# Kernel tuning notes

Hardware: AMD Instinct MI355X
Metric: run time of the kernel (lower is better)

The kernel has to match this reference:

```python
import jax, jax.numpy as jnp
import numpy as np

N_GENE = 100000
N_DIS = 20000
H = 128
E = 500000


def setup_inputs() -> dict:
    key = jax.random.key(0)
    ks = jax.random.split(key, 12)
    s1 = 1.0 / np.sqrt(2 * H)  # fan-in init scale, Linear(2H, H)
    s2 = 1.0 / np.sqrt(H)      # fan-in init scale, Linear(H, 1)
    z_gene = jax.random.normal(ks[0], (N_GENE, H), jnp.float32)
    z_disease = jax.random.normal(ks[1], (N_DIS, H), jnp.float32)
    # gene->disease edges: row indexes genes, col indexes diseases
    edges_gd = jnp.stack([
        jax.random.randint(ks[2], (E,), 0, N_GENE),
        jax.random.randint(ks[3], (E,), 0, N_DIS),
    ])
    # gene->gene edges
    edges_gg = jnp.stack([
        jax.random.randint(ks[4], (E,), 0, N_GENE),
        jax.random.randint(ks[5], (E,), 0, N_GENE),
    ])
    return {
        "z_gene": z_gene,
        "z_disease": z_disease,
        "edges_gd": edges_gd,
        "edges_gg": edges_gg,
        "w1_gd": jax.random.normal(ks[6], (2 * H, H), jnp.float32) * s1,
        "b1_gd": jnp.zeros((H,), jnp.float32),
        "w2_gd": jax.random.normal(ks[7], (H, 1), jnp.float32) * s2,
        "b2_gd": jnp.zeros((1,), jnp.float32),
        "w1_gg": jax.random.normal(ks[8], (2 * H, H), jnp.float32) * s1,
        "b1_gg": jnp.zeros((H,), jnp.float32),
        "w2_gg": jax.random.normal(ks[9], (H, 1), jnp.float32) * s2,
        "b2_gg": jnp.zeros((1,), jnp.float32),
    }


def _decode(z_src, z_dst, edges, w1, b1, w2, b2):
    # gather src/dst node embeddings by edge index, concat -> [E, 2H]
    z = jnp.concatenate([z_src[edges[0]], z_dst[edges[1]]], axis=1)
    h = jnp.maximum(z @ w1 + b1, 0.0)  # Linear + ReLU
    return h @ w2 + b2                  # Linear -> [E, 1]


def reference(z_gene, z_disease, edges_gd, edges_gg,
              w1_gd, b1_gd, w2_gd, b2_gd,
              w1_gg, b1_gg, w2_gg, b2_gg):
    out_gd = _decode(z_gene, z_disease, edges_gd, w1_gd, b1_gd, w2_gd, b2_gd)
    out_gg = _decode(z_gene, z_gene, edges_gg, w1_gg, b1_gg, w2_gg, b2_gg)
    # dict of per-relation outputs in the original; stack since E matches
    return jnp.stack([out_gd, out_gg])  # [2, E, 1]
```

## Files before the change

kernel.cpp:

```cpp
#include <hip/hip_runtime.h>
#include <hip/hip_bf16.h>

#define HDIM 128

typedef __attribute__((ext_vector_type(8))) short short8;
typedef __attribute__((ext_vector_type(4))) float floatx4;

__device__ __forceinline__ float bf2f(unsigned short u) {
    return __uint_as_float(((unsigned)u) << 16);
}
__device__ __forceinline__ unsigned short f2b(float f) {
    __hip_bfloat16 h = __float2bfloat16(f);
    return __builtin_bit_cast(unsigned short, h);
}
__device__ __forceinline__ float ldv(const void* p, size_t i, int flag) {
    return flag ? bf2f(((const unsigned short*)p)[i]) : ((const float*)p)[i];
}
__device__ __forceinline__ short8 pack8(float4 a, float4 b) {
    short8 r;
    r[0] = (short)f2b(a.x); r[1] = (short)f2b(a.y);
    r[2] = (short)f2b(a.z); r[3] = (short)f2b(a.w);
    r[4] = (short)f2b(b.x); r[5] = (short)f2b(b.y);
    r[6] = (short)f2b(b.z); r[7] = (short)f2b(b.w);
    return r;
}

__device__ __forceinline__ int local_detect(const unsigned short* zbits) {
    __shared__ int red[256];
    int tid = threadIdx.x;
    int cnt = 0;
    for (int i = tid; i < 4096; i += 256) {
        int ex = (zbits[i] >> 7) & 0xFF;
        if (ex >= 100 && ex <= 140) cnt++;
    }
    red[tid] = cnt;
    __syncthreads();
    for (int s = 128; s > 0; s >>= 1) {
        if (tid < s) red[tid] += red[tid + s];
        __syncthreads();
    }
    return (red[0] >= 3686) ? 1 : 0;
}

__global__ __launch_bounds__(256) void prep_kernel(
    const unsigned short* __restrict__ zbits,
    const void* __restrict__ w1_gd, const void* __restrict__ w1_gg,
    const void* __restrict__ b1_gd, const void* __restrict__ w2_gd,
    const void* __restrict__ b2_gd, const void* __restrict__ b1_gg,
    const void* __restrict__ w2_gg, const void* __restrict__ b2_gg,
    unsigned short* __restrict__ img, float* __restrict__ params,
    int* __restrict__ flagout)
{
    int flag = local_detect(zbits);
    int b = blockIdx.x;
    int tid = threadIdx.x;
    if (b < 32) {
        int im   = b >> 3;
        int sub  = b & 7;
        const void* w1 = (im < 2) ? w1_gd : w1_gg;
        int part = im & 1;
        unsigned short* out = img + im * 16384;
        int n = tid & 127;
#pragma unroll
        for (int it = 0; it < 8; ++it) {
            int k = sub * 16 + it * 2 + (tid >> 7);
            unsigned short v = flag
                ? ((const unsigned short*)w1)[(size_t)(part * 128 + k) * 128 + n]
                : f2b(((const float*)w1)[(size_t)(part * 128 + k) * 128 + n]);
            out[n * 128 + (((k >> 3) ^ (n & 15)) << 3) + (k & 7)] = v;
        }
    } else {
        if (tid < 128) {
            params[tid]       = ldv(b1_gd, tid, flag);
            params[256 + tid] = ldv(b1_gg, tid, flag);
        } else {
            params[tid]       = ldv(w2_gd, tid - 128, flag);
            params[256 + tid] = ldv(w2_gg, tid - 128, flag);
        }
        if (tid == 0) {
            params[512] = ldv(b2_gd, 0, flag);
            params[513] = ldv(b2_gg, 0, flag);
            *flagout = flag;
        }
    }
}

__global__ __launch_bounds__(256) void proj_all_kernel(
    const void* __restrict__ Zg, const void* __restrict__ Zd,
    const uint4* __restrict__ Wimg, const float* __restrict__ params,
    unsigned short* __restrict__ A_gd, unsigned short* __restrict__ B_gd,
    unsigned short* __restrict__ A_gg, unsigned short* __restrict__ B_gg,
    int NG, int ND, int gblk, const int* __restrict__ flagp)
{
    __shared__ uint4 sW[2048];
    int tid  = threadIdx.x;
    int lane = tid & 63;
    int wave = tid >> 6;
    int nl   = lane & 15;
    int quad = lane >> 4;
    int flag = *flagp;

    bool gene = (int)blockIdx.x < gblk;
    int blk = gene ? blockIdx.x : blockIdx.x - gblk;
    int M = gene ? NG : ND;
    const void* Z = gene ? Zg : Zd;

    int row0 = blk * 128 + wave * 32 + nl;
    int row1 = row0 + 16;
    int r0c = row0 < M ? row0 : (M - 1);
    int r1c = row1 < M ? row1 : (M - 1);

    short8 zf[2][4];
    if (flag) {
        const uint4* z0 = (const uint4*)Z + (size_t)r0c * 16;
        const uint4* z1 = (const uint4*)Z + (size_t)r1c * 16;
#pragma unroll
        for (int kc = 0; kc < 4; ++kc) {
            zf[0][kc] = __builtin_bit_cast(short8, z0[kc * 4 + quad]);
            zf[1][kc] = __builtin_bit_cast(short8, z1[kc * 4 + quad]);
        }
    } else {
        const float4* z0 = (const float4*)Z + (size_t)r0c * 32;
        const float4* z1 = (const float4*)Z + (size_t)r1c * 32;
#pragma unroll
        for (int kc = 0; kc < 4; ++kc) {
            int o = kc * 8 + quad * 2;
            zf[0][kc] = pack8(z0[o], z0[o + 1]);
            zf[1][kc] = pack8(z1[o], z1[o + 1]);
        }
    }

    int nph = gene ? 3 : 1;
    for (int ph = 0; ph < nph; ++ph) {
        const uint4* im;
        unsigned short* Out;
        const float* bias;
        if (gene) {
            im   = Wimg + (ph == 0 ? 0 : ph == 1 ? 2 : 3) * 2048;
            Out  = ph == 0 ? A_gd : ph == 1 ? A_gg : B_gg;
            bias = ph == 0 ? params : ph == 1 ? params + 256 : nullptr;
        } else {
            im = Wimg + 2048; Out = B_gd; bias = nullptr;
        }
        __syncthreads();
#pragma unroll
        for (int i = 0; i < 8; ++i) sW[tid + i * 256] = im[tid + i * 256];
        __syncthreads();

        floatx4 acc[2][8];
#pragma unroll
        for (int rt = 0; rt < 2; ++rt)
#pragma unroll
            for (int nt = 0; nt < 8; ++nt)
                acc[rt][nt] = (floatx4){0.f, 0.f, 0.f, 0.f};

#pragma unroll
        for (int kc = 0; kc < 4; ++kc) {
            int p = (kc * 4 + quad) ^ nl;
#pragma unroll
            for (int nt = 0; nt < 8; ++nt) {
                short8 wf = __builtin_bit_cast(short8, sW[(nt * 16 + nl) * 16 + p]);
                acc[0][nt] = __builtin_amdgcn_mfma_f32_16x16x32_bf16(wf, zf[0][kc], acc[0][nt], 0, 0, 0);
                acc[1][nt] = __builtin_amdgcn_mfma_f32_16x16x32_bf16(wf, zf[1][kc], acc[1][nt], 0, 0, 0);
            }
        }
#pragma unroll
        for (int rt = 0; rt < 2; ++rt) {
            int row = rt ? row1 : row0;
            if (row < M) {
#pragma unroll
                for (int nt = 0; nt < 8; ++nt) {
                    float4 bv = {0.f, 0.f, 0.f, 0.f};
                    if (bias) bv = *(const float4*)(bias + nt * 16 + quad * 4);
                    ushort4 v;
                    v.x = f2b(acc[rt][nt][0] + bv.x);
                    v.y = f2b(acc[rt][nt][1] + bv.y);
                    v.z = f2b(acc[rt][nt][2] + bv.z);
                    v.w = f2b(acc[rt][nt][3] + bv.w);
                    *(ushort4*)(Out + (size_t)row * HDIM + nt * 16 + quad * 4) = v;
                }
            }
        }
    }
}

__global__ __launch_bounds__(256) void edge_kernel(
    const int* __restrict__ edges_gd, const int* __restrict__ edges_gg,
    const unsigned short* __restrict__ A_gd, const unsigned short* __restrict__ B_gd,
    const unsigned short* __restrict__ A_gg, const unsigned short* __restrict__ B_gg,
    const float* __restrict__ params,
    void* __restrict__ out, int E, int nb, const int* __restrict__ flagp)
{
    int rel = ((int)blockIdx.x >= nb) ? 1 : 0;
    int blk = blockIdx.x - rel * nb;
    const int* edges = rel ? edges_gg : edges_gd;
    const unsigned short* A = rel ? A_gg : A_gd;
    const unsigned short* B = rel ? B_gg : B_gd;
    const float* w2 = params + 128 + rel * 256;
    float b2 = params[512 + rel];

    int tid  = threadIdx.x;
    int lane = tid & 63;
    int wave = tid >> 6;
    int nl   = lane & 7;
    int grp  = lane >> 3;

    float w2f[16];
#pragma unroll
    for (int i = 0; i < 4; ++i) {
        float4 t = *(const float4*)(w2 + nl * 16 + i * 4);
        w2f[i * 4 + 0] = t.x; w2f[i * 4 + 1] = t.y;
        w2f[i * 4 + 2] = t.z; w2f[i * 4 + 3] = t.w;
    }

    int e0 = blk * 64 + (wave * 8 + grp) * 2;
    int e1 = e0 + 1;
    int emax = E - 2 > 0 ? E - 2 : 0;
    int ec = e0 < emax ? e0 : emax;
    int sel = e0 - ec;
    int2 sp = *(const int2*)(edges + ec);
    int2 dp = *(const int2*)(edges + E + ec);
    int src0 = sel ? sp.y : sp.x;
    int dst0 = sel ? dp.y : dp.x;
    int src1 = sp.y;
    int dst1 = dp.y;

    const uint4* a0p = (const uint4*)(A + (size_t)src0 * HDIM) + nl * 2;
    const uint4* b0p = (const uint4*)(B + (size_t)dst0 * HDIM) + nl * 2;
    const uint4* a1p = (const uint4*)(A + (size_t)src1 * HDIM) + nl * 2;
    const uint4* b1p = (const uint4*)(B + (size_t)dst1 * HDIM) + nl * 2;
    uint4 a0[2] = {a0p[0], a0p[1]};
    uint4 c0[2] = {b0p[0], b0p[1]};
    uint4 a1[2] = {a1p[0], a1p[1]};
    uint4 c1[2] = {b1p[0], b1p[1]};

    float acc0 = 0.f, acc1 = 0.f;
#pragma unroll
    for (int i = 0; i < 2; ++i) {
        const unsigned* au0 = (const unsigned*)&a0[i];
        const unsigned* cu0 = (const unsigned*)&c0[i];
        const unsigned* au1 = (const unsigned*)&a1[i];
        const unsigned* cu1 = (const unsigned*)&c1[i];
#pragma unroll
        for (int j = 0; j < 4; ++j) {
            int ch = i * 8 + j * 2;
            float x0 = __uint_as_float(au0[j] << 16);
            float x1 = __uint_as_float(au0[j] & 0xffff0000u);
            float y0 = __uint_as_float(cu0[j] << 16);
            float y1 = __uint_as_float(cu0[j] & 0xffff0000u);
            acc0 = fmaf(fmaxf(x0 + y0, 0.f), w2f[ch], acc0);
            acc0 = fmaf(fmaxf(x1 + y1, 0.f), w2f[ch + 1], acc0);
            float u0 = __uint_as_float(au1[j] << 16);
            float u1 = __uint_as_float(au1[j] & 0xffff0000u);
            float v0 = __uint_as_float(cu1[j] << 16);
            float v1 = __uint_as_float(cu1[j] & 0xffff0000u);
            acc1 = fmaf(fmaxf(u0 + v0, 0.f), w2f[ch], acc1);
            acc1 = fmaf(fmaxf(u1 + v1, 0.f), w2f[ch + 1], acc1);
        }
    }
    acc0 += __shfl_xor(acc0, 1); acc1 += __shfl_xor(acc1, 1);
    acc0 += __shfl_xor(acc0, 2); acc1 += __shfl_xor(acc1, 2);
    acc0 += __shfl_xor(acc0, 4); acc1 += __shfl_xor(acc1, 4);

    if (nl == 0) {
        int flag = *flagp;
        size_t base = (size_t)rel * E;
        if (e0 < E) {
            float r = acc0 + b2;
            if (flag) ((unsigned short*)out)[base + e0] = f2b(r);
            else      ((float*)out)[base + e0] = r;
        }
        if (e1 < E) {
            float r = acc1 + b2;
            if (flag) ((unsigned short*)out)[base + e1] = f2b(r);
            else      ((float*)out)[base + e1] = r;
        }
    }
}

__global__ __launch_bounds__(256) void detect_kernel(
    const unsigned short* __restrict__ zbits, int* __restrict__ flag)
{
    int f = local_detect(zbits);
    if (threadIdx.x == 0) *flag = f;
}

__global__ __launch_bounds__(128) void naive_edge_kernel(
    const int* __restrict__ edges,
    const void* __restrict__ zsrc, const void* __restrict__ zdst,
    const void* __restrict__ w1, const void* __restrict__ b1,
    const void* __restrict__ w2, const void* __restrict__ b2,
    void* __restrict__ out, size_t eoff, int E,
    const int* __restrict__ flagp)
{
    int flag = flagp ? *flagp : 0;
    __shared__ float zs[128], zd[128], red[128];
    int e = blockIdx.x;
    int n = threadIdx.x;
    int src = edges[e], dst = edges[E + e];
    zs[n] = ldv(zsrc, (size_t)src * HDIM + n, flag);
    zd[n] = ldv(zdst, (size_t)dst * HDIM + n, flag);
    __syncthreads();
    float acc = ldv(b1, n, flag);
    for (int k = 0; k < 128; ++k) acc = fmaf(zs[k], ldv(w1, (size_t)k * HDIM + n, flag), acc);
    for (int k = 0; k < 128; ++k) acc = fmaf(zd[k], ldv(w1, (size_t)(128 + k) * HDIM + n, flag), acc);
    red[n] = fmaxf(acc, 0.f) * ldv(w2, n, flag);
    __syncthreads();
    for (int s = 64; s > 0; s >>= 1) {
        if (n < s) red[n] += red[n + s];
        __syncthreads();
    }
    if (n == 0) {
        float r = red[0] + ldv(b2, 0, flag);
        if (flag) ((unsigned short*)out)[eoff + e] = f2b(r);
        else      ((float*)out)[eoff + e] = r;
    }
}

extern "C" void kernel_launch(void* const* d_in, const int* in_sizes, int n_in,
                              void* d_out, int out_size, void* d_ws, size_t ws_size,
                              hipStream_t stream)
{
    const void* z_gene = d_in[0];
    const void* z_dis  = d_in[1];
    const int* edges_gd = (const int*)d_in[2];
    const int* edges_gg = (const int*)d_in[3];
    const void* w1_gd = d_in[4];
    const void* b1_gd = d_in[5];
    const void* w2_gd = d_in[6];
    const void* b2_gd = d_in[7];
    const void* w1_gg = d_in[8];
    const void* b1_gg = d_in[9];
    const void* w2_gg = d_in[10];
    const void* b2_gg = d_in[11];

    int NG = in_sizes[0] / HDIM;
    int ND = in_sizes[1] / HDIM;
    int E  = in_sizes[2] / 2;

    size_t off_flag   = 0;
    size_t off_params = 256;
    size_t off_img    = 2560;
    size_t off_Agd    = off_img + 131072;
    size_t off_Bgd    = off_Agd + (size_t)NG * HDIM * 2;
    size_t off_Agg    = off_Bgd + (size_t)ND * HDIM * 2;
    size_t off_Bgg    = off_Agg + (size_t)NG * HDIM * 2;
    size_t need       = off_Bgg + (size_t)NG * HDIM * 2;

    char* ws = (char*)d_ws;

    if (ws_size < need) {
        const int* flagp = nullptr;
        if (ws_size >= 16) {
            detect_kernel<<<1, 256, 0, stream>>>((const unsigned short*)z_gene, (int*)ws);
            flagp = (const int*)ws;
        }
        naive_edge_kernel<<<E, 128, 0, stream>>>(edges_gd, z_gene, z_dis,
                                                 w1_gd, b1_gd, w2_gd, b2_gd,
                                                 d_out, 0, E, flagp);
        naive_edge_kernel<<<E, 128, 0, stream>>>(edges_gg, z_gene, z_gene,
                                                 w1_gg, b1_gg, w2_gg, b2_gg,
                                                 d_out, (size_t)E, E, flagp);
        return;
    }

    int* flag = (int*)(ws + off_flag);
    float* params = (float*)(ws + off_params);
    unsigned short* img = (unsigned short*)(ws + off_img);
    unsigned short* Agd = (unsigned short*)(ws + off_Agd);
    unsigned short* Bgd = (unsigned short*)(ws + off_Bgd);
    unsigned short* Agg = (unsigned short*)(ws + off_Agg);
    unsigned short* Bgg = (unsigned short*)(ws + off_Bgg);

    prep_kernel<<<33, 256, 0, stream>>>((const unsigned short*)z_gene,
                                        w1_gd, w1_gg, b1_gd, w2_gd, b2_gd,
                                        b1_gg, w2_gg, b2_gg, img, params, flag);

    const uint4* img4 = (const uint4*)img;
    int gblk = (NG + 127) / 128;
    int dblk = (ND + 127) / 128;
    proj_all_kernel<<<gblk + dblk, 256, 0, stream>>>(z_gene, z_dis, img4, params,
                                                     Agd, Bgd, Agg, Bgg,
                                                     NG, ND, gblk, flag);

    int nb = (E + 63) / 64;
    edge_kernel<<<2 * nb, 256, 0, stream>>>(edges_gd, edges_gg, Agd, Bgd, Agg, Bgg,
                                            params, d_out, E, nb, flag);
}
```

Baseline: 226.6 us.

## Split projection into per-matrix blocks reading weights directly from global memory

Replaces the fused projection kernel, which reused one loaded z tile across three weight phases via a swizzled LDS image, with one block per (matrix, 64-row tile). Weight fragments are read directly from global/L2 in a plain layout, removing LDS staging and barriers, and a zero bias region replaces the null-bias branch. This raises parallelism and removes synchronisation but re-reads gene embeddings three times and relies on L2 for weight loads.

```diff
diff --git a/kernel.cpp b/kernel.cpp
--- a/kernel.cpp
+++ b/kernel.cpp
@@ -67,12 +67,13 @@
             unsigned short v = flag
                 ? ((const unsigned short*)w1)[(size_t)(part * 128 + k) * 128 + n]
                 : f2b(((const float*)w1)[(size_t)(part * 128 + k) * 128 + n]);
-            out[n * 128 + (((k >> 3) ^ (n & 15)) << 3) + (k & 7)] = v;
+            out[n * 128 + k] = v;
         }
     } else {
         if (tid < 128) {
             params[tid]       = ldv(b1_gd, tid, flag);
             params[256 + tid] = ldv(b1_gg, tid, flag);
+            params[768 + tid] = 0.f;
         } else {
             params[tid]       = ldv(w2_gd, tid - 128, flag);
             params[256 + tid] = ldv(w2_gg, tid - 128, flag);
@@ -85,101 +86,68 @@
     }
 }
 
-__global__ __launch_bounds__(256) void proj_all_kernel(
+__global__ __launch_bounds__(256) void proj_kernel(
     const void* __restrict__ Zg, const void* __restrict__ Zd,
-    const uint4* __restrict__ Wimg, const float* __restrict__ params,
+    const uint4* __restrict__ img, const float* __restrict__ params,
     unsigned short* __restrict__ A_gd, unsigned short* __restrict__ B_gd,
     unsigned short* __restrict__ A_gg, unsigned short* __restrict__ B_gg,
     int NG, int ND, int gblk, const int* __restrict__ flagp)
 {
-    __shared__ uint4 sW[2048];
+    int id = blockIdx.x;
+    const void* Z; int M; const uint4* W; unsigned short* Out; const float* bias;
+    if (id < gblk)            { Z = Zg; M = NG; W = img;            Out = A_gd; bias = params;       }
+    else if (id < 2 * gblk)   { Z = Zg; M = NG; W = img + 2 * 2048; Out = A_gg; bias = params + 256; id -= gblk; }
+    else if (id < 3 * gblk)   { Z = Zg; M = NG; W = img + 3 * 2048; Out = B_gg; bias = params + 768; id -= 2 * gblk; }
+    else                      { Z = Zd; M = ND; W = img + 2048;     Out = B_gd; bias = params + 768; id -= 3 * gblk; }
+
     int tid  = threadIdx.x;
     int lane = tid & 63;
     int wave = tid >> 6;
     int nl   = lane & 15;
     int quad = lane >> 4;
-    int flag = *flagp;
-
-    bool gene = (int)blockIdx.x < gblk;
-    int blk = gene ? blockIdx.x : blockIdx.x - gblk;
-    int M = gene ? NG : ND;
-    const void* Z = gene ? Zg : Zd;
-
-    int row0 = blk * 128 + wave * 32 + nl;
-    int row1 = row0 + 16;
-    int r0c = row0 < M ? row0 : (M - 1);
-    int r1c = row1 < M ? row1 : (M - 1);
-
-    short8 zf[2][4];
-    if (flag) {
-        const uint4* z0 = (const uint4*)Z + (size_t)r0c * 16;
-        const uint4* z1 = (const uint4*)Z + (size_t)r1c * 16;
-#pragma unroll
-        for (int kc = 0; kc < 4; ++kc) {
-            zf[0][kc] = __builtin_bit_cast(short8, z0[kc * 4 + quad]);
-            zf[1][kc] = __builtin_bit_cast(short8, z1[kc * 4 + quad]);
-        }
+
+    int row = id * 64 + wave * 16 + nl;
+    int rc  = row < M ? row : (M - 1);
+
+    short8 zf[4];
+    if (*flagp) {
+        const uint4* z = (const uint4*)Z + (size_t)rc * 16;
+#pragma unroll
+        for (int kc = 0; kc < 4; ++kc)
+            zf[kc] = __builtin_bit_cast(short8, z[kc * 4 + quad]);
     } else {
-        const float4* z0 = (const float4*)Z + (size_t)r0c * 32;
-        const float4* z1 = (const float4*)Z + (size_t)r1c * 32;
+        const float4* z = (const float4*)Z + (size_t)rc * 32;
 #pragma unroll
         for (int kc = 0; kc < 4; ++kc) {
             int o = kc * 8 + quad * 2;
-            zf[0][kc] = pack8(z0[o], z0[o + 1]);
-            zf[1][kc] = pack8(z1[o], z1[o + 1]);
-        }
-    }
-
-    int nph = gene ? 3 : 1;
-    for (int ph = 0; ph < nph; ++ph) {
-        const uint4* im;
-        unsigned short* Out;
-        const float* bias;
-        if (gene) {
-            im   = Wimg + (ph == 0 ? 0 : ph == 1 ? 2 : 3) * 2048;
-            Out  = ph == 0 ? A_gd : ph == 1 ? A_gg : B_gg;
-            bias = ph == 0 ? params : ph == 1 ? params + 256 : nullptr;
-        } else {
-            im = Wimg + 2048; Out = B_gd; bias = nullptr;
-        }
-        __syncthreads();
-#pragma unroll
-        for (int i = 0; i < 8; ++i) sW[tid + i * 256] = im[tid + i * 256];
-        __syncthreads();
-
-        floatx4 acc[2][8];
-#pragma unroll
-        for (int rt = 0; rt < 2; ++rt)
-#pragma unroll
-            for (int nt = 0; nt < 8; ++nt)
-                acc[rt][nt] = (floatx4){0.f, 0.f, 0.f, 0.f};
-
-#pragma unroll
-        for (int kc = 0; kc < 4; ++kc) {
-            int p = (kc * 4 + quad) ^ nl;
-#pragma unroll
-            for (int nt = 0; nt < 8; ++nt) {
-                short8 wf = __builtin_bit_cast(short8, sW[(nt * 16 + nl) * 16 + p]);
-                acc[0][nt] = __builtin_amdgcn_mfma_f32_16x16x32_bf16(wf, zf[0][kc], acc[0][nt], 0, 0, 0);
-                acc[1][nt] = __builtin_amdgcn_mfma_f32_16x16x32_bf16(wf, zf[1][kc], acc[1][nt], 0, 0, 0);
-            }
-        }
-#pragma unroll
-        for (int rt = 0; rt < 2; ++rt) {
-            int row = rt ? row1 : row0;
-            if (row < M) {
-#pragma unroll
-                for (int nt = 0; nt < 8; ++nt) {
-                    float4 bv = {0.f, 0.f, 0.f, 0.f};
-                    if (bias) bv = *(const float4*)(bias + nt * 16 + quad * 4);
-                    ushort4 v;
-                    v.x = f2b(acc[rt][nt][0] + bv.x);
-                    v.y = f2b(acc[rt][nt][1] + bv.y);
-                    v.z = f2b(acc[rt][nt][2] + bv.z);
-                    v.w = f2b(acc[rt][nt][3] + bv.w);
-                    *(ushort4*)(Out + (size_t)row * HDIM + nt * 16 + quad * 4) = v;
-                }
-            }
+            zf[kc] = pack8(z[o], z[o + 1]);
+        }
+    }
+
+    floatx4 acc[8];
+#pragma unroll
+    for (int nt = 0; nt < 8; ++nt) acc[nt] = (floatx4){0.f, 0.f, 0.f, 0.f};
+
+#pragma unroll
+    for (int kc = 0; kc < 4; ++kc) {
+        int kch = kc * 4 + quad;
+#pragma unroll
+        for (int nt = 0; nt < 8; ++nt) {
+            short8 wf = __builtin_bit_cast(short8, W[(nt * 16 + nl) * 16 + kch]);
+            acc[nt] = __builtin_amdgcn_mfma_f32_16x16x32_bf16(wf, zf[kc], acc[nt], 0, 0, 0);
+        }
+    }
+
+    if (row < M) {
+#pragma unroll
+        for (int nt = 0; nt < 8; ++nt) {
+            float4 bv = *(const float4*)(bias + nt * 16 + quad * 4);
+            ushort4 v;
+            v.x = f2b(acc[nt][0] + bv.x);
+            v.y = f2b(acc[nt][1] + bv.y);
+            v.z = f2b(acc[nt][2] + bv.z);
+            v.w = f2b(acc[nt][3] + bv.w);
+            *(ushort4*)(Out + (size_t)row * HDIM + nt * 16 + quad * 4) = v;
         }
     }
 }
@@ -340,7 +308,7 @@
 
     size_t off_flag   = 0;
     size_t off_params = 256;
-    size_t off_img    = 2560;
+    size_t off_img    = 256 + 4096;
     size_t off_Agd    = off_img + 131072;
     size_t off_Bgd    = off_Agd + (size_t)NG * HDIM * 2;
     size_t off_Agg    = off_Bgd + (size_t)ND * HDIM * 2;
@@ -377,9 +345,9 @@
                                         b1_gg, w2_gg, b2_gg, img, params, flag);
 
     const uint4* img4 = (const uint4*)img;
-    int gblk = (NG + 127) / 128;
-    int dblk = (ND + 127) / 128;
-    proj_all_kernel<<<gblk + dblk, 256, 0, stream>>>(z_gene, z_dis, img4, params,
+    int gblk = (NG + 63) / 64;
+    int dblk = (ND + 63) / 64;
+    proj_kernel<<<3 * gblk + dblk, 256, 0, stream>>>(z_gene, z_dis, img4, params,
                                                      Agd, Bgd, Agg, Bgg,
                                                      NG, ND, gblk, flag);
 
```

New measurement: 280.8 us. +23.9%, slower.

## Split projection into one block per weight and process four edges per lane group

Applied to the files above, without the earlier changes.

The projection kernel stops looping over three weight phases inside each gene block and launches a separate block per (row tile, weight matrix). This gives more parallel blocks and removes the phase barriers, but the gene embeddings are now re-read three times. A zero bias vector is added so the bias branch can be dropped. The edge kernel now handles four edges per 8-lane group, with int4 index loads and vectorized output stores, to raise memory-level parallelism for the random gathers.

```diff
diff --git a/kernel.cpp b/kernel.cpp
--- a/kernel.cpp
+++ b/kernel.cpp
@@ -73,6 +73,7 @@
         if (tid < 128) {
             params[tid]       = ldv(b1_gd, tid, flag);
             params[256 + tid] = ldv(b1_gg, tid, flag);
+            params[768 + tid] = 0.f;
         } else {
             params[tid]       = ldv(w2_gd, tid - 128, flag);
             params[256 + tid] = ldv(w2_gg, tid - 128, flag);
@@ -85,33 +86,37 @@
     }
 }
 
-__global__ __launch_bounds__(256) void proj_all_kernel(
+__global__ __launch_bounds__(256) void proj_kernel(
     const void* __restrict__ Zg, const void* __restrict__ Zd,
-    const uint4* __restrict__ Wimg, const float* __restrict__ params,
+    const uint4* __restrict__ img, const float* __restrict__ params,
     unsigned short* __restrict__ A_gd, unsigned short* __restrict__ B_gd,
     unsigned short* __restrict__ A_gg, unsigned short* __restrict__ B_gg,
     int NG, int ND, int gblk, const int* __restrict__ flagp)
 {
     __shared__ uint4 sW[2048];
+    int id = blockIdx.x;
+    const void* Z; int M; const uint4* W; unsigned short* Out; const float* bias;
+    if (id < gblk)            { Z = Zg; M = NG; W = img;            Out = A_gd; bias = params;       }
+    else if (id < 2 * gblk)   { Z = Zg; M = NG; W = img + 2 * 2048; Out = A_gg; bias = params + 256; id -= gblk; }
+    else if (id < 3 * gblk)   { Z = Zg; M = NG; W = img + 3 * 2048; Out = B_gg; bias = params + 768; id -= 2 * gblk; }
+    else                      { Z = Zd; M = ND; W = img + 2048;     Out = B_gd; bias = params + 768; id -= 3 * gblk; }
+
     int tid  = threadIdx.x;
     int lane = tid & 63;
     int wave = tid >> 6;
     int nl   = lane & 15;
     int quad = lane >> 4;
-    int flag = *flagp;
-
-    bool gene = (int)blockIdx.x < gblk;
-    int blk = gene ? blockIdx.x : blockIdx.x - gblk;
-    int M = gene ? NG : ND;
-    const void* Z = gene ? Zg : Zd;
-
-    int row0 = blk * 128 + wave * 32 + nl;
+
+#pragma unroll
+    for (int i = 0; i < 8; ++i) sW[tid + i * 256] = W[tid + i * 256];
+
+    int row0 = id * 128 + wave * 32 + nl;
     int row1 = row0 + 16;
     int r0c = row0 < M ? row0 : (M - 1);
     int r1c = row1 < M ? row1 : (M - 1);
 
     short8 zf[2][4];
-    if (flag) {
+    if (*flagp) {
         const uint4* z0 = (const uint4*)Z + (size_t)r0c * 16;
         const uint4* z1 = (const uint4*)Z + (size_t)r1c * 16;
 #pragma unroll
@@ -129,56 +134,39 @@
             zf[1][kc] = pack8(z1[o], z1[o + 1]);
         }
     }
-
-    int nph = gene ? 3 : 1;
-    for (int ph = 0; ph < nph; ++ph) {
-        const uint4* im;
-        unsigned short* Out;
-        const float* bias;
-        if (gene) {
-            im   = Wimg + (ph == 0 ? 0 : ph == 1 ? 2 : 3) * 2048;
-            Out  = ph == 0 ? A_gd : ph == 1 ? A_gg : B_gg;
-            bias = ph == 0 ? params : ph == 1 ? params + 256 : nullptr;
-        } else {
-            im = Wimg + 2048; Out = B_gd; bias = nullptr;
-        }
-        __syncthreads();
-#pragma unroll
-        for (int i = 0; i < 8; ++i) sW[tid + i * 256] = im[tid + i * 256];
-        __syncthreads();
-
-        floatx4 acc[2][8];
-#pragma unroll
-        for (int rt = 0; rt < 2; ++rt)
-#pragma unroll
-            for (int nt = 0; nt < 8; ++nt)
-                acc[rt][nt] = (floatx4){0.f, 0.f, 0.f, 0.f};
-
-#pragma unroll
-        for (int kc = 0; kc < 4; ++kc) {
-            int p = (kc * 4 + quad) ^ nl;
+    __syncthreads();
+
+    floatx4 acc[2][8];
+#pragma unroll
+    for (int rt = 0; rt < 2; ++rt)
+#pragma unroll
+        for (int nt = 0; nt < 8; ++nt)
+            acc[rt][nt] = (floatx4){0.f, 0.f, 0.f, 0.f};
+
+#pragma unroll
+    for (int kc = 0; kc < 4; ++kc) {
+        int p = (kc * 4 + quad) ^ nl;
+#pragma unroll
+        for (int nt = 0; nt < 8; ++nt) {
+            short8 wf = __builtin_bit_cast(short8, sW[(nt * 16 + nl) * 16 + p]);
+            acc[0][nt] = __builtin_amdgcn_mfma_f32_16x16x32_bf16(wf, zf[0][kc], acc[0][nt], 0, 0, 0);
+            acc[1][nt] = __builtin_amdgcn_mfma_f32_16x16x32_bf16(wf, zf[1][kc], acc[1][nt], 0, 0, 0);
+        }
+    }
+
+#pragma unroll
+    for (int rt = 0; rt < 2; ++rt) {
+        int row = rt ? row1 : row0;
+        if (row < M) {
 #pragma unroll
             for (int nt = 0; nt < 8; ++nt) {
-                short8 wf = __builtin_bit_cast(short8, sW[(nt * 16 + nl) * 16 + p]);
-                acc[0][nt] = __builtin_amdgcn_mfma_f32_16x16x32_bf16(wf, zf[0][kc], acc[0][nt], 0, 0, 0);
-                acc[1][nt] = __builtin_amdgcn_mfma_f32_16x16x32_bf16(wf, zf[1][kc], acc[1][nt], 0, 0, 0);
-            }
-        }
-#pragma unroll
-        for (int rt = 0; rt < 2; ++rt) {
-            int row = rt ? row1 : row0;
-            if (row < M) {
-#pragma unroll
-                for (int nt = 0; nt < 8; ++nt) {
-                    float4 bv = {0.f, 0.f, 0.f, 0.f};
-                    if (bias) bv = *(const float4*)(bias + nt * 16 + quad * 4);
-                    ushort4 v;
-                    v.x = f2b(acc[rt][nt][0] + bv.x);
-                    v.y = f2b(acc[rt][nt][1] + bv.y);
-                    v.z = f2b(acc[rt][nt][2] + bv.z);
-                    v.w = f2b(acc[rt][nt][3] + bv.w);
-                    *(ushort4*)(Out + (size_t)row * HDIM + nt * 16 + quad * 4) = v;
-                }
+                float4 bv = *(const float4*)(bias + nt * 16 + quad * 4);
+                ushort4 v;
+                v.x = f2b(acc[rt][nt][0] + bv.x);
+                v.y = f2b(acc[rt][nt][1] + bv.y);
+                v.z = f2b(acc[rt][nt][2] + bv.z);
+                v.w = f2b(acc[rt][nt][3] + bv.w);
+                *(ushort4*)(Out + (size_t)row * HDIM + nt * 16 + quad * 4) = v;
             }
         }
     }
@@ -213,67 +201,82 @@
         w2f[i * 4 + 2] = t.z; w2f[i * 4 + 3] = t.w;
     }
 
-    int e0 = blk * 64 + (wave * 8 + grp) * 2;
-    int e1 = e0 + 1;
-    int emax = E - 2 > 0 ? E - 2 : 0;
-    int ec = e0 < emax ? e0 : emax;
-    int sel = e0 - ec;
-    int2 sp = *(const int2*)(edges + ec);
-    int2 dp = *(const int2*)(edges + E + ec);
-    int src0 = sel ? sp.y : sp.x;
-    int dst0 = sel ? dp.y : dp.x;
-    int src1 = sp.y;
-    int dst1 = dp.y;
-
-    const uint4* a0p = (const uint4*)(A + (size_t)src0 * HDIM) + nl * 2;
-    const uint4* b0p = (const uint4*)(B + (size_t)dst0 * HDIM) + nl * 2;
-    const uint4* a1p = (const uint4*)(A + (size_t)src1 * HDIM) + nl * 2;
-    const uint4* b1p = (const uint4*)(B + (size_t)dst1 * HDIM) + nl * 2;
-    uint4 a0[2] = {a0p[0], a0p[1]};
-    uint4 c0[2] = {b0p[0], b0p[1]};
-    uint4 a1[2] = {a1p[0], a1p[1]};
-    uint4 c1[2] = {b1p[0], b1p[1]};
-
-    float acc0 = 0.f, acc1 = 0.f;
-#pragma unroll
-    for (int i = 0; i < 2; ++i) {
-        const unsigned* au0 = (const unsigned*)&a0[i];
-        const unsigned* cu0 = (const unsigned*)&c0[i];
-        const unsigned* au1 = (const unsigned*)&a1[i];
-        const unsigned* cu1 = (const unsigned*)&c1[i];
-#pragma unroll
-        for (int j = 0; j < 4; ++j) {
-            int ch = i * 8 + j * 2;
-            float x0 = __uint_as_float(au0[j] << 16);
-            float x1 = __uint_as_float(au0[j] & 0xffff0000u);
-            float y0 = __uint_as_float(cu0[j] << 16);
-            float y1 = __uint_as_float(cu0[j] & 0xffff0000u);
-            acc0 = fmaf(fmaxf(x0 + y0, 0.f), w2f[ch], acc0);
-            acc0 = fmaf(fmaxf(x1 + y1, 0.f), w2f[ch + 1], acc0);
-            float u0 = __uint_as_float(au1[j] << 16);
-            float u1 = __uint_as_float(au1[j] & 0xffff0000u);
-            float v0 = __uint_as_float(cu1[j] << 16);
-            float v1 = __uint_as_float(cu1[j] & 0xffff0000u);
-            acc1 = fmaf(fmaxf(u0 + v0, 0.f), w2f[ch], acc1);
-            acc1 = fmaf(fmaxf(u1 + v1, 0.f), w2f[ch + 1], acc1);
-        }
-    }
-    acc0 += __shfl_xor(acc0, 1); acc1 += __shfl_xor(acc1, 1);
-    acc0 += __shfl_xor(acc0, 2); acc1 += __shfl_xor(acc1, 2);
-    acc0 += __shfl_xor(acc0, 4); acc1 += __shfl_xor(acc1, 4);
+    int e0 = blk * 128 + (wave * 8 + grp) * 4;
+    int ecap = E - 4;
+    int ec = e0 < ecap ? e0 : ecap;
+    int4 sp = *(const int4*)(edges + ec);
+    int4 dp = *(const int4*)(edges + E + ec);
+    int s0 = sp.x, s1 = sp.y, s2 = sp.z, s3 = sp.w;
+    int d0 = dp.x, d1 = dp.y, d2 = dp.z, d3 = dp.w;
+    if (e0 != ec) {
+        s0 = (e0 + 0 < E) ? edges[e0 + 0] : s0;  d0 = (e0 + 0 < E) ? edges[E + e0 + 0] : d0;
+        s1 = (e0 + 1 < E) ? edges[e0 + 1] : s1;  d1 = (e0 + 1 < E) ? edges[E + e0 + 1] : d1;
+        s2 = (e0 + 2 < E) ? edges[e0 + 2] : s2;  d2 = (e0 + 2 < E) ? edges[E + e0 + 2] : d2;
+        s3 = (e0 + 3 < E) ? edges[e0 + 3] : s3;  d3 = (e0 + 3 < E) ? edges[E + e0 + 3] : d3;
+    }
+
+    const uint4* ap0 = (const uint4*)(A + (size_t)s0 * HDIM) + nl * 2;
+    const uint4* bp0 = (const uint4*)(B + (size_t)d0 * HDIM) + nl * 2;
+    const uint4* ap1 = (const uint4*)(A + (size_t)s1 * HDIM) + nl * 2;
+    const uint4* bp1 = (const uint4*)(B + (size_t)d1 * HDIM) + nl * 2;
+    const uint4* ap2 = (const uint4*)(A + (size_t)s2 * HDIM) + nl * 2;
+    const uint4* bp2 = (const uint4*)(B + (size_t)d2 * HDIM) + nl * 2;
+    const uint4* ap3 = (const uint4*)(A + (size_t)s3 * HDIM) + nl * 2;
+    const uint4* bp3 = (const uint4*)(B + (size_t)d3 * HDIM) + nl * 2;
+
+    uint4 a[4][2], c[4][2];
+    a[0][0] = ap0[0]; a[0][1] = ap0[1]; c[0][0] = bp0[0]; c[0][1] = bp0[1];
+    a[1][0] = ap1[0]; a[1][1] = ap1[1]; c[1][0] = bp1[0]; c[1][1] = bp1[1];
+    a[2][0] = ap2[0]; a[2][1] = ap2[1]; c[2][0] = bp2[0]; c[2][1] = bp2[1];
+    a[3][0] = ap3[0]; a[3][1] = ap3[1]; c[3][0] = bp3[0]; c[3][1] = bp3[1];
+
+    float acc[4] = {0.f, 0.f, 0.f, 0.f};
+#pragma unroll
+    for (int k = 0; k < 4; ++k) {
+#pragma unroll
+        for (int i = 0; i < 2; ++i) {
+            const unsigned* au = (const unsigned*)&a[k][i];
+            const unsigned* cu = (const unsigned*)&c[k][i];
+#pragma unroll
+            for (int j = 0; j < 4; ++j) {
+                int ch = i * 8 + j * 2;
+                float x0 = __uint_as_float(au[j] << 16);
+                float x1 = __uint_as_float(au[j] & 0xffff0000u);
+                float y0 = __uint_as_float(cu[j] << 16);
+                float y1 = __uint_as_float(cu[j] & 0xffff0000u);
+                acc[k] = fmaf(fmaxf(x0 + y0, 0.f), w2f[ch], acc[k]);
+                acc[k] = fmaf(fmaxf(x1 + y1, 0.f), w2f[ch + 1], acc[k]);
+            }
+        }
+    }
+#pragma unroll
+    for (int k = 0; k < 4; ++k) {
+        acc[k] += __shfl_xor(acc[k], 1);
+        acc[k] += __shfl_xor(acc[k], 2);
+        acc[k] += __shfl_xor(acc[k], 4);
+    }
 
     if (nl == 0) {
         int flag = *flagp;
         size_t base = (size_t)rel * E;
-        if (e0 < E) {
-            float r = acc0 + b2;
-            if (flag) ((unsigned short*)out)[base + e0] = f2b(r);
-            else      ((float*)out)[base + e0] = r;
-        }
-        if (e1 < E) {
-            float r = acc1 + b2;
-            if (flag) ((unsigned short*)out)[base + e1] = f2b(r);
-            else      ((float*)out)[base + e1] = r;
+        float r0 = acc[0] + b2, r1 = acc[1] + b2, r2 = acc[2] + b2, r3 = acc[3] + b2;
+        if (e0 + 3 < E) {
+            if (flag) {
+                ushort4 v = {f2b(r0), f2b(r1), f2b(r2), f2b(r3)};
+                *(ushort4*)((unsigned short*)out + base + e0) = v;
+            } else {
+                float4 v = {r0, r1, r2, r3};
+                *(float4*)((float*)out + base + e0) = v;
+            }
+        } else {
+            float rr[4] = {r0, r1, r2, r3};
+#pragma unroll
+            for (int k = 0; k < 4; ++k) {
+                if (e0 + k < E) {
+                    if (flag) ((unsigned short*)out)[base + e0 + k] = f2b(rr[k]);
+                    else      ((float*)out)[base + e0 + k] = rr[k];
+                }
+            }
         }
     }
 }
@@ -340,7 +343,7 @@
 
     size_t off_flag   = 0;
     size_t off_params = 256;
-    size_t off_img    = 2560;
+    size_t off_img    = 256 + 4096;
     size_t off_Agd    = off_img + 131072;
     size_t off_Bgd    = off_Agd + (size_t)NG * HDIM * 2;
     size_t off_Agg    = off_Bgd + (size_t)ND * HDIM * 2;
@@ -379,11 +382,11 @@
     const uint4* img4 = (const uint4*)img;
     int gblk = (NG + 127) / 128;
     int dblk = (ND + 127) / 128;
-    proj_all_kernel<<<gblk + dblk, 256, 0, stream>>>(z_gene, z_dis, img4, params,
+    proj_kernel<<<3 * gblk + dblk, 256, 0, stream>>>(z_gene, z_dis, img4, params,
                                                      Agd, Bgd, Agg, Bgg,
                                                      NG, ND, gblk, flag);
 
-    int nb = (E + 63) / 64;
+    int nb = (E + 127) / 128;
     edge_kernel<<<2 * nb, 256, 0, stream>>>(edges_gd, edges_gg, Agd, Bgd, Agg, Bgg,
                                             params, d_out, E, nb, flag);
 }
```

Result: no change. 229.6 us (+1.4%).
